# Optimization experiments

Hardware: AMD Instinct MI355X
Metric: run time of the kernel (lower is better)

The kernel has to match this reference:

```python
import jax, jax.numpy as jnp
import numpy as np

N = 20000      # num nodes
E = 200000     # num edges (no self loops; GATConv adds them)
ND = 128       # node_feature_dim
ED = 64        # edge_feature_dim
H = 256        # hidden_dim (= GAT out_channels per head, concat=False)
HEADS = 4
L = 3          # num_gnn_layers


def setup_inputs() -> dict:
    key = jax.random.key(0)
    ks = jax.random.split(key, 24)
    rng = np.random.default_rng(0)
    src = rng.integers(0, N, size=E)
    dst = (src + 1 + rng.integers(0, N - 1, size=E)) % N  # guaranteed no self loops
    edge_index = jnp.asarray(np.stack([src, dst]), dtype=jnp.int32)
    s = 0.05
    inp = {
        'node_features': jax.random.normal(ks[0], (N, ND), jnp.float32),
        'edge_attr': jax.random.normal(ks[1], (E, ED), jnp.float32),
        'enc_w': jax.random.normal(ks[2], (ND, H), jnp.float32) * s,
        'enc_b': jnp.zeros((H,), jnp.float32),
        'edge_enc_w': jax.random.normal(ks[3], (L, ED, H), jnp.float32) * s,
        'edge_enc_b': jnp.zeros((L, H), jnp.float32),
        'gat_w': jax.random.normal(ks[4], (L, H, HEADS * H), jnp.float32) * s,
        'att_src': jax.random.normal(ks[5], (L, HEADS, H), jnp.float32) * s,
        'att_dst': jax.random.normal(ks[6], (L, HEADS, H), jnp.float32) * s,
        'att_edge': jax.random.normal(ks[7], (L, HEADS, H), jnp.float32) * s,
        'lin_edge_w': jax.random.normal(ks[8], (L, 1, HEADS * H), jnp.float32) * s,
        'gat_b': jnp.zeros((L, H), jnp.float32),
        'ln_g': jnp.ones((L, H), jnp.float32),
        'ln_b': jnp.zeros((L, H), jnp.float32),
        'head_w1': jax.random.normal(ks[9], (4, H, H // 2), jnp.float32) * s,
        'head_b1': jnp.zeros((4, H // 2), jnp.float32),
        'head_w2': jax.random.normal(ks[10], (4, H // 2, 1), jnp.float32) * s,
        'head_b2': jnp.zeros((4, 1), jnp.float32),
        'edge_index': edge_index,
    }
    return inp


def _layernorm(x, g, b, eps=1e-5):
    mu = x.mean(-1, keepdims=True)
    v = ((x - mu) ** 2).mean(-1, keepdims=True)
    return g * (x - mu) / jnp.sqrt(v + eps) + b


def _gat_layer(x, src, dst, ew_full, w, a_s_vec, a_d_vec, a_e_vec, lew, bias):
    # x: [N,H]; GATConv(heads=4, concat=False) with scalar edge feature (edge_dim=1)
    xp = (x @ w).reshape(N, HEADS, H)                       # [N,HEADS,H]
    a_s = (xp * a_s_vec).sum(-1)                            # [N,HEADS]
    a_d = (xp * a_d_vec).sum(-1)                            # [N,HEADS]
    ef = (ew_full[:, None] @ lew).reshape(-1, HEADS, H)     # [Etot,HEADS,H]
    a_e = (ef * a_e_vec).sum(-1)                            # [Etot,HEADS]
    logits = jax.nn.leaky_relu(a_s[src] + a_d[dst] + a_e, 0.2)
    m = jax.ops.segment_max(logits, dst, num_segments=N)    # segment softmax over dst
    p = jnp.exp(logits - m[dst])
    ssum = jax.ops.segment_sum(p, dst, num_segments=N)
    alpha = p / ssum[dst]                                   # [Etot,HEADS]
    out = jax.ops.segment_sum(alpha[:, :, None] * xp[src], dst, num_segments=N)
    return out.mean(1) + bias                               # concat=False -> mean over heads


def reference(node_features, edge_attr, enc_w, enc_b, edge_enc_w, edge_enc_b,
              gat_w, att_src, att_dst, att_edge, lin_edge_w, gat_b,
              ln_g, ln_b, head_w1, head_b1, head_w2, head_b2, edge_index):
    src0, dst0 = edge_index[0], edge_index[1]
    loop = jnp.arange(N, dtype=edge_index.dtype)
    src = jnp.concatenate([src0, loop])   # self loops appended (GATConv add_self_loops)
    dst = jnp.concatenate([dst0, loop])
    deg = jax.ops.segment_sum(jnp.ones((E,), node_features.dtype), dst0, num_segments=N)

    x = jax.nn.relu(node_features @ enc_w + enc_b)          # node encoder (dropout: eval)
    for l in range(L):
        ew = (edge_attr @ edge_enc_w[l] + edge_enc_b[l]).mean(-1)  # [E] scalar edge weight
        loop_w = jax.ops.segment_sum(ew, dst0, num_segments=N) / jnp.maximum(deg, 1.0)
        ew_full = jnp.concatenate([ew, loop_w])             # fill_value='mean' for self loops
        h = _gat_layer(x, src, dst, ew_full, gat_w[l], att_src[l], att_dst[l],
                       att_edge[l], lin_edge_w[l], gat_b[l])
        h = _layernorm(h, ln_g[l], ln_b[l])
        x = jax.nn.relu(x + h)
    emb = x                                                 # [N,H]

    # 4 prediction heads vectorized: k in {attrition, engagement, collaboration, anomaly}
    hmid = jax.nn.relu(jnp.einsum('nd,kdh->knh', emb, head_w1) + head_b1[:, None, :])
    o = jnp.einsum('knh,kho->kno', hmid, head_w2) + head_b2[:, None, :]  # [4,N,1]
    attrition = jax.nn.sigmoid(o[0])
    engagement = o[1]
    collaboration = o[2]
    anomaly = jax.nn.sigmoid(o[3])
    return (attrition, engagement, collaboration, anomaly, emb)
```

## Files before the change

### kernel.cpp

```cpp
#include <hip/hip_runtime.h>
#include <math.h>

#define N_NODES 20000
#define N_EDGES 200000
#define NDIM 128
#define EDIM 64
#define HDIM 256
#define HEADS 4
#define NH 1024
#define NLAYERS 3

typedef __attribute__((ext_vector_type(8))) short short8;
typedef __attribute__((ext_vector_type(4))) float floatx4;

__device__ __forceinline__ float b2f(unsigned short u) {
    union { unsigned u; float f; } c; c.u = ((unsigned)u) << 16; return c.f;
}
__device__ __forceinline__ float b2f_lo(unsigned u) {
    union { unsigned u; float f; } c; c.u = u << 16; return c.f;
}
__device__ __forceinline__ float b2f_hi(unsigned u) {
    union { unsigned u; float f; } c; c.u = u & 0xffff0000u; return c.f;
}
__device__ __forceinline__ unsigned short f2b(float f) {
    union { float f; unsigned u; } c; c.f = f;
    unsigned u = c.u;
    return (unsigned short)((u + 0x7FFFu + ((u >> 16) & 1u)) >> 16);
}
__device__ __forceinline__ float lrelu(float v) { return v > 0.f ? v : 0.2f * v; }

__global__ void hist_kernel(const int* __restrict__ dst0, int* __restrict__ cnt) {
    int e = blockIdx.x * 256 + threadIdx.x;
    if (e < N_EDGES) atomicAdd(&cnt[dst0[e]], 1);
}

__global__ __launch_bounds__(1024) void scan_full(const int* __restrict__ cnt,
                                                  int* __restrict__ row_ptr) {
    const int PER = 20;
    __shared__ int wtot[16];
    int t = threadIdx.x, lane = t & 63, wid = t >> 6;
    int base = t * PER;
    int loc[PER];
    int s = 0;
    #pragma unroll
    for (int i = 0; i < PER; i++) {
        int idx = base + i;
        int v = (idx < N_NODES) ? cnt[idx] : 0;
        loc[i] = s; s += v;
    }
    int inc = s;
    #pragma unroll
    for (int off = 1; off < 64; off <<= 1) {
        int tt = __shfl_up(inc, off, 64);
        if (lane >= off) inc += tt;
    }
    if (lane == 63) wtot[wid] = inc;
    __syncthreads();
    int woff = 0;
    #pragma unroll
    for (int w = 0; w < 16; w++) if (w < wid) woff += wtot[w];
    int excl = woff + inc - s;
    #pragma unroll
    for (int i = 0; i < PER; i++) {
        int idx = base + i;
        if (idx < N_NODES) row_ptr[idx] = excl + loc[i];
    }
    if (t == 1023) row_ptr[N_NODES] = excl + s;
}

__global__ __launch_bounds__(256) void fill_ew(const int* __restrict__ src0,
                                               const int* __restrict__ dst0,
                                               const float* __restrict__ edge_attr,
                                               const float* __restrict__ wmean3,
                                               const float* __restrict__ scal3,
                                               const int* __restrict__ row_ptr,
                                               int* __restrict__ fillc,
                                               int* __restrict__ srcCSR,
                                               float* __restrict__ ewCSR4) {
    int e = blockIdx.x * 256 + threadIdx.x;
    if (e >= N_EDGES) return;
    int d = dst0[e];
    int p = atomicAdd(&fillc[d], 1);
    int pos = row_ptr[d] + p;
    srcCSR[pos] = src0[e];
    const float* row = edge_attr + (size_t)e * EDIM;
    float s0 = 0.f, s1 = 0.f, s2 = 0.f;
    #pragma unroll
    for (int dd = 0; dd < EDIM; dd += 4) {
        float4 a  = *(const float4*)(row + dd);
        float4 w0 = *(const float4*)(wmean3 + dd);
        float4 w1 = *(const float4*)(wmean3 + 64 + dd);
        float4 w2 = *(const float4*)(wmean3 + 128 + dd);
        s0 += a.x * w0.x + a.y * w0.y + a.z * w0.z + a.w * w0.w;
        s1 += a.x * w1.x + a.y * w1.y + a.z * w1.z + a.w * w1.w;
        s2 += a.x * w2.x + a.y * w2.y + a.z * w2.z + a.w * w2.w;
    }
    *(float4*)(ewCSR4 + (size_t)pos * 4) =
        make_float4(s0 + scal3[4], s1 + scal3[12], s2 + scal3[20], 0.f);
}

#define PC_CONV   2500
#define PC_TENC   (PC_CONV + 32)
#define PC_GWP    (PC_TENC + 768)
#define PC_WSP    (PC_GWP + 12)
#define PC_THW1   (PC_WSP + 128)
#define PC_TOTAL  (PC_THW1 + 3)

__device__ void transpose_body(const float* in, unsigned short* out, int K, int Nn,
                               int bx, int by, float sh[32][33], float scale) {
    int tid = threadIdx.x;
    int tx = tid & 31, ty = tid >> 5;
    int kb = by * 32, nb = bx * 32;
    #pragma unroll
    for (int i = 0; i < 32; i += 8)
        sh[ty + i][tx] = in[(size_t)(kb + ty + i) * Nn + nb + tx];
    __syncthreads();
    #pragma unroll
    for (int i = 0; i < 32; i += 8)
        out[(size_t)(nb + ty + i) * K + kb + tx] = f2b(scale * sh[tx][ty + i]);
}

__global__ __launch_bounds__(256) void prep_combo(
    const float* __restrict__ node_features, unsigned short* __restrict__ nf_bf,
    const float* __restrict__ enc_w, unsigned short* __restrict__ enc_wt,
    const float* __restrict__ gat_w, unsigned short* __restrict__ gw2t,
    const float* __restrict__ att_src, const float* __restrict__ att_dst,
    float* __restrict__ ws_s, float* __restrict__ ws_d,
    const float* __restrict__ head_w1, unsigned short* __restrict__ hw1t,
    const float* __restrict__ edge_enc_w, const float* __restrict__ edge_enc_b,
    const float* __restrict__ lin_edge_w, const float* __restrict__ att_edge,
    float* __restrict__ wmean3, float* __restrict__ scal3)
{
    __shared__ float sh[32][33];
    int b = blockIdx.x;
    int tid = threadIdx.x;
    if (b < PC_CONV) {
        int i = b * 256 + tid;
        float4 v = ((const float4*)node_features)[i];
        ushort4 o;
        o.x = f2b(v.x); o.y = f2b(v.y); o.z = f2b(v.z); o.w = f2b(v.w);
        ((ushort4*)nf_bf)[i] = o;
    } else if (b < PC_TENC) {
        int b2 = b - PC_CONV;
        transpose_body(enc_w, enc_wt, NDIM, HDIM, b2 & 7, b2 >> 3, sh, 1.f);
    } else if (b < PC_GWP) {
        int b3 = b - PC_TENC;
        int bx = b3 & 7, by = (b3 >> 3) & 7, z = b3 >> 6;
        int l = z >> 2, h = z & 3;
        const float* src = gat_w + (size_t)l * HDIM * NH + (size_t)h * HDIM;
        unsigned short* dst = gw2t + (size_t)l * HDIM * NH + (size_t)h * HDIM;
        int tx = tid & 31, ty = tid >> 5;
        int kb = by * 32, db = bx * 32;
        #pragma unroll
        for (int i = 0; i < 32; i += 8)
            sh[ty + i][tx] = src[(size_t)(kb + ty + i) * NH + db + tx];
        __syncthreads();
        #pragma unroll
        for (int i = 0; i < 32; i += 8)
            dst[(size_t)(db + ty + i) * NH + kb + tx] = f2b(0.25f * sh[tx][ty + i]);
    } else if (b < PC_WSP) {
        int bx = b - PC_GWP;
        int l = bx >> 2, h = bx & 3;
        int k = tid;
        const float* wrow = gat_w + (size_t)l * HDIM * NH + (size_t)k * NH + h * HDIM;
        const float* as = att_src + (size_t)l * NH + h * HDIM;
        const float* ad = att_dst + (size_t)l * NH + h * HDIM;
        float s1 = 0.f, s2 = 0.f;
        for (int d = 0; d < HDIM; d += 4) {
            float4 w4 = *(const float4*)(wrow + d);
            float4 a4 = *(const float4*)(as + d);
            float4 b4 = *(const float4*)(ad + d);
            s1 += w4.x * a4.x + w4.y * a4.y + w4.z * a4.z + w4.w * a4.w;
            s2 += w4.x * b4.x + w4.y * b4.y + w4.z * b4.z + w4.w * b4.w;
        }
        ws_s[(size_t)bx * HDIM + k] = s1;
        ws_d[(size_t)bx * HDIM + k] = s2;
    } else if (b < PC_THW1) {
        int b4 = b - PC_WSP;
        int bx = b4 & 3, by = (b4 >> 2) & 7, z = b4 >> 5;
        transpose_body(head_w1 + (size_t)z * HDIM * 128,
                       hw1t + (size_t)z * 128 * HDIM, HDIM, 128, bx, by, sh, 1.f);
    } else {
        int l = b - PC_THW1;
        const float* eew = edge_enc_w + (size_t)l * EDIM * HDIM;
        const float* eeb = edge_enc_b + (size_t)l * HDIM;
        const float* lew = lin_edge_w + (size_t)l * NH;
        const float* ae  = att_edge + (size_t)l * NH;
        float* wm = wmean3 + l * 64;
        float* sc = scal3 + l * 8;
        if (tid < 64) {
            float s = 0.f;
            for (int d = 0; d < HDIM; d++) s += eew[tid * HDIM + d];
            wm[tid] = s * (1.f / HDIM);
        } else if (tid < 68) {
            int h = tid - 64;
            float s = 0.f;
            for (int d = 0; d < HDIM; d++) s += lew[h * HDIM + d] * ae[h * HDIM + d];
            sc[h] = s;
        } else if (tid == 68) {
            float s = 0.f;
            for (int d = 0; d < HDIM; d++) s += eeb[d];
            sc[4] = s * (1.f / HDIM);
        }
    }
}

template <bool RELU, bool BIAS>
__global__ __launch_bounds__(256) void gemm_bf16(
    const unsigned short* __restrict__ A, const unsigned short* __restrict__ Bt,
    const float* __restrict__ bias, unsigned short* __restrict__ C,
    int M, int Ntot, int K)
{
    __shared__ char lds[24576];
    unsigned short* As = (unsigned short*)lds;
    unsigned short* Bs = (unsigned short*)(lds + 8192);
    unsigned short* Cs = (unsigned short*)lds;

    int Cb = Ntot >> 7;
    int P  = (M + 63) >> 6;
    int d  = blockIdx.x;
    int xcd = d & 7;
    int i5  = d >> 3;
    int p   = xcd + 8 * (i5 / Cb);
    int cblk = i5 % Cb;
    if (p >= P) return;
    int row0 = p * 64;
    int col0 = cblk * 128;

    int tid = threadIdx.x;
    int lane = tid & 63;
    int wid = tid >> 6;
    int wm = (wid >> 1) * 32;
    int wn = (wid & 1) * 64;
    int lm = lane & 15;
    int q8 = (lane >> 4) * 8;
    int q4 = (lane >> 4) * 4;

    floatx4 acc[2][4];
    #pragma unroll
    for (int i = 0; i < 2; i++)
        #pragma unroll
        for (int j = 0; j < 4; j++)
            acc[i][j] = (floatx4)(0.f);

    int arow = tid >> 2;
    int acol = (tid & 3) * 8;
    int garow = row0 + arow; if (garow > M - 1) garow = M - 1;

    for (int k0 = 0; k0 < K; k0 += 64) {
        #pragma unroll
        for (int kk = 0; kk < 2; kk++) {
            int kb = k0 + kk * 32;
            __builtin_amdgcn_global_load_lds(
                (__attribute__((address_space(1))) const void*)(A + (size_t)garow * K + kb + acol),
                (__attribute__((address_space(3))) void*)(As + kk * 2048 + tid * 8), 16, 0, 0);
            #pragma unroll
            for (int r = 0; r < 2; r++) {
                int chunk = tid + r * 256;
                int brow = chunk >> 2;
                int bcol = (chunk & 3) * 8;
                __builtin_amdgcn_global_load_lds(
                    (__attribute__((address_space(1))) const void*)(Bt + (size_t)(col0 + brow) * K + kb + bcol),
                    (__attribute__((address_space(3))) void*)(Bs + kk * 4096 + chunk * 8), 16, 0, 0);
            }
        }
        __syncthreads();
        #pragma unroll
        for (int kk = 0; kk < 2; kk++) {
            short8 af[2], bf[4];
            #pragma unroll
            for (int i = 0; i < 2; i++)
                af[i] = *(const short8*)(As + kk * 2048 + (wm + i * 16 + lm) * 32 + q8);
            #pragma unroll
            for (int j = 0; j < 4; j++)
                bf[j] = *(const short8*)(Bs + kk * 4096 + (wn + j * 16 + lm) * 32 + q8);
            #pragma unroll
            for (int i = 0; i < 2; i++)
                #pragma unroll
                for (int j = 0; j < 4; j++)
                    acc[i][j] = __builtin_amdgcn_mfma_f32_16x16x32_bf16(af[i], bf[j], acc[i][j], 0, 0, 0);
        }
        __syncthreads();
    }

    #pragma unroll
    for (int i = 0; i < 2; i++) {
        #pragma unroll
        for (int j = 0; j < 4; j++) {
            int cl = wn + j * 16 + lm;
            float bv = BIAS ? bias[col0 + cl] : 0.f;
            #pragma unroll
            for (int reg = 0; reg < 4; reg++) {
                int rl = wm + i * 16 + q4 + reg;
                float v = acc[i][j][reg];
                if (BIAS) v += bv;
                if (RELU) v = fmaxf(v, 0.f);
                Cs[rl * 128 + cl] = f2b(v);
            }
        }
    }
    __syncthreads();
    int row = tid >> 2;
    int seg = (tid & 3) * 32;
    if (row0 + row < M) {
        #pragma unroll
        for (int u = 0; u < 4; u++) {
            int4 v = *(const int4*)(Cs + row * 128 + seg + u * 8);
            *(int4*)(C + (size_t)(row0 + row) * Ntot + col0 + seg + u * 8) = v;
        }
    }
}

__global__ __launch_bounds__(256) void gemm_head(
    const unsigned short* __restrict__ A, const unsigned short* __restrict__ Bt,
    const float* __restrict__ bias, int M, int Ntot, int K,
    const float* __restrict__ w2, const float* __restrict__ b2v,
    float* __restrict__ outp)
{
    __shared__ char lds[24576];
    unsigned short* As = (unsigned short*)lds;
    unsigned short* Bs = (unsigned short*)(lds + 8192);
    unsigned short* Cs = (unsigned short*)lds;

    int Cb = Ntot >> 7;
    int P  = (M + 63) >> 6;
    int d  = blockIdx.x;
    int xcd = d & 7;
    int i5  = d >> 3;
    int p   = xcd + 8 * (i5 / Cb);
    int cblk = i5 % Cb;
    if (p >= P) return;
    int row0 = p * 64;
    int col0 = cblk * 128;

    int tid = threadIdx.x;
    int lane = tid & 63;
    int wid = tid >> 6;
    int wm = (wid >> 1) * 32;
    int wn = (wid & 1) * 64;
    int lm = lane & 15;
    int q8 = (lane >> 4) * 8;
    int q4 = (lane >> 4) * 4;

    floatx4 acc[2][4];
    #pragma unroll
    for (int i = 0; i < 2; i++)
        #pragma unroll
        for (int j = 0; j < 4; j++)
            acc[i][j] = (floatx4)(0.f);

    int arow = tid >> 2;
    int acol = (tid & 3) * 8;
    int garow = row0 + arow; if (garow > M - 1) garow = M - 1;

    for (int k0 = 0; k0 < K; k0 += 64) {
        #pragma unroll
        for (int kk = 0; kk < 2; kk++) {
            int kb = k0 + kk * 32;
            __builtin_amdgcn_global_load_lds(
                (__attribute__((address_space(1))) const void*)(A + (size_t)garow * K + kb + acol),
                (__attribute__((address_space(3))) void*)(As + kk * 2048 + tid * 8), 16, 0, 0);
            #pragma unroll
            for (int r = 0; r < 2; r++) {
                int chunk = tid + r * 256;
                int brow = chunk >> 2;
                int bcol = (chunk & 3) * 8;
                __builtin_amdgcn_global_load_lds(
                    (__attribute__((address_space(1))) const void*)(Bt + (size_t)(col0 + brow) * K + kb + bcol),
                    (__attribute__((address_space(3))) void*)(Bs + kk * 4096 + chunk * 8), 16, 0, 0);
            }
        }
        __syncthreads();
        #pragma unroll
        for (int kk = 0; kk < 2; kk++) {
            short8 af[2], bf[4];
            #pragma unroll
            for (int i = 0; i < 2; i++)
                af[i] = *(const short8*)(As + kk * 2048 + (wm + i * 16 + lm) * 32 + q8);
            #pragma unroll
            for (int j = 0; j < 4; j++)
                bf[j] = *(const short8*)(Bs + kk * 4096 + (wn + j * 16 + lm) * 32 + q8);
            #pragma unroll
            for (int i = 0; i < 2; i++)
                #pragma unroll
                for (int j = 0; j < 4; j++)
                    acc[i][j] = __builtin_amdgcn_mfma_f32_16x16x32_bf16(af[i], bf[j], acc[i][j], 0, 0, 0);
        }
        __syncthreads();
    }

    #pragma unroll
    for (int i = 0; i < 2; i++) {
        #pragma unroll
        for (int j = 0; j < 4; j++) {
            int cl = wn + j * 16 + lm;
            float bv = bias[col0 + cl];
            #pragma unroll
            for (int reg = 0; reg < 4; reg++) {
                int rl = wm + i * 16 + q4 + reg;
                float v = fmaxf(acc[i][j][reg] + bv, 0.f);
                Cs[rl * 128 + cl] = f2b(v);
            }
        }
    }
    __syncthreads();
    int row = tid >> 2;
    int seg = (tid & 3) * 32;
    int k = col0 >> 7;
    const float* wr = w2 + k * 128;
    const unsigned short* cr = Cs + row * 128 + seg;
    float s = 0.f;
    #pragma unroll
    for (int u = 0; u < 4; u++) {
        int4 v = *(const int4*)(cr + u * 8);
        float4 w0 = *(const float4*)(wr + seg + u * 8);
        float4 w1 = *(const float4*)(wr + seg + u * 8 + 4);
        s += b2f_lo((unsigned)v.x) * w0.x + b2f_hi((unsigned)v.x) * w0.y
           + b2f_lo((unsigned)v.y) * w0.z + b2f_hi((unsigned)v.y) * w0.w;
        s += b2f_lo((unsigned)v.z) * w1.x + b2f_hi((unsigned)v.z) * w1.y
           + b2f_lo((unsigned)v.w) * w1.z + b2f_hi((unsigned)v.w) * w1.w;
    }
    s += __shfl_xor(s, 1, 64);
    s += __shfl_xor(s, 2, 64);
    if ((tid & 3) == 0 && row0 + row < M) {
        s += b2v[k];
        if (k == 0 || k == 3) s = 1.f / (1.f + __expf(-s));
        outp[(size_t)k * N_NODES + row0 + row] = s;
    }
}

__global__ __launch_bounds__(256) void attn_x(const unsigned short* __restrict__ x_bf,
                                              const float* __restrict__ ws_s,
                                              const float* __restrict__ ws_d,
                                              float* __restrict__ a_s,
                                              float* __restrict__ a_d)
{
    int wid = threadIdx.x >> 6, lane = threadIdx.x & 63;
    int n = blockIdx.x * 4 + wid;
    ushort4 xv = *(const ushort4*)(x_bf + (size_t)n * HDIM + lane * 4);
    float x0 = b2f(xv.x), x1 = b2f(xv.y), x2 = b2f(xv.z), x3 = b2f(xv.w);
    float ss[4], sd[4];
    #pragma unroll
    for (int h = 0; h < 4; h++) {
        float4 s4 = *(const float4*)(ws_s + h * HDIM + lane * 4);
        float4 d4 = *(const float4*)(ws_d + h * HDIM + lane * 4);
        ss[h] = x0 * s4.x + x1 * s4.y + x2 * s4.z + x3 * s4.w;
        sd[h] = x0 * d4.x + x1 * d4.y + x2 * d4.z + x3 * d4.w;
    }
    #pragma unroll
    for (int off = 32; off > 0; off >>= 1)
        #pragma unroll
        for (int h = 0; h < 4; h++) {
            ss[h] += __shfl_xor(ss[h], off, 64);
            sd[h] += __shfl_xor(sd[h], off, 64);
        }
    if (lane == 0) {
        *(float4*)(a_s + n * 4) = make_float4(ss[0], ss[1], ss[2], ss[3]);
        *(float4*)(a_d + n * 4) = make_float4(sd[0], sd[1], sd[2], sd[3]);
    }
}

__global__ __launch_bounds__(256) void gat_agg_fused(
    const unsigned short* __restrict__ x_bf, const float* __restrict__ a_s,
    const float* __restrict__ a_d,
    const float* __restrict__ scal, const int* __restrict__ row_ptr,
    const int* __restrict__ srcCSR, const float* __restrict__ ewCSR4,
    int l, unsigned short* __restrict__ agg)
{
    int wid = threadIdx.x >> 6, lane = threadIdx.x & 63;
    int n = blockIdx.x * 4 + wid;
    int r0 = row_ptr[n];
    int deg = row_ptr[n + 1] - r0;
    int cnt = deg + 1;

    float4 c4 = *(const float4*)scal;
    float4 as4 = *(const float4*)(a_s + (size_t)n * 4);
    float4 ad4 = *(const float4*)(a_d + (size_t)n * 4);

    int sv0 = n; float w0 = 0.f;
    if (lane < deg) {
        sv0 = srcCSR[r0 + lane];
        w0 = ewCSR4[(((size_t)(r0 + lane)) << 2) + l];
    }
    float sw = w0;
    for (int c0 = 64; c0 < deg; c0 += 64) {
        int i2 = c0 + lane;
        if (i2 < deg) sw += ewCSR4[(((size_t)(r0 + i2)) << 2) + l];
    }
    #pragma unroll
    for (int off = 32; off > 0; off >>= 1) sw += __shfl_xor(sw, off, 64);
    float lw = sw / fmaxf((float)deg, 1.f);

    float4 zself;
    zself.x = lrelu(as4.x + ad4.x + c4.x * lw);
    zself.y = lrelu(as4.y + ad4.y + c4.y * lw);
    zself.z = lrelu(as4.z + ad4.z + c4.z * lw);
    zself.w = lrelu(as4.w + ad4.w + c4.w * lw);

    auto comp_z = [&](int c0, int& sv, float4& z) {
        int ix = c0 + lane;
        if (ix < deg) {
            sv = srcCSR[r0 + ix];
            float w = ewCSR4[(((size_t)(r0 + ix)) << 2) + l];
            float4 zs = *(const float4*)(a_s + (size_t)sv * 4);
            z.x = lrelu(zs.x + ad4.x + c4.x * w);
            z.y = lrelu(zs.y + ad4.y + c4.y * w);
            z.z = lrelu(zs.z + ad4.z + c4.z * w);
            z.w = lrelu(zs.w + ad4.w + c4.w * w);
        } else if (ix == deg) {
            sv = n; z = zself;
        } else {
            sv = n; z.x = z.y = z.z = z.w = -1e30f;
        }
    };

    float4 z0;
    if (lane < deg) {
        float4 zs = *(const float4*)(a_s + (size_t)sv0 * 4);
        z0.x = lrelu(zs.x + ad4.x + c4.x * w0);
        z0.y = lrelu(zs.y + ad4.y + c4.y * w0);
        z0.z = lrelu(zs.z + ad4.z + c4.z * w0);
        z0.w = lrelu(zs.w + ad4.w + c4.w * w0);
    } else if (lane == deg) {
        z0 = zself;
    } else {
        z0.x = z0.y = z0.z = z0.w = -1e30f;
    }

    float4 p0;
    p0.x = __expf(z0.x); p0.y = __expf(z0.y);
    p0.z = __expf(z0.z); p0.w = __expf(z0.w);
    float s0 = p0.x, s1 = p0.y, s2 = p0.z, s3 = p0.w;
    for (int c0 = 64; c0 < cnt; c0 += 64) {
        int sv; float4 z; comp_z(c0, sv, z);
        s0 += __expf(z.x); s1 += __expf(z.y);
        s2 += __expf(z.z); s3 += __expf(z.w);
    }
    #pragma unroll
    for (int off = 32; off > 0; off >>= 1) {
        s0 += __shfl_xor(s0, off, 64);
        s1 += __shfl_xor(s1, off, 64);
        s2 += __shfl_xor(s2, off, 64);
        s3 += __shfl_xor(s3, off, 64);
    }
    float i0 = 1.f / s0, i1 = 1.f / s1, i2 = 1.f / s2, i3 = 1.f / s3;
    float4 al0;
    al0.x = p0.x * i0; al0.y = p0.y * i1; al0.z = p0.z * i2; al0.w = p0.w * i3;

    float acc[4][4] = {};
    const unsigned short* xw = x_bf + (size_t)lane * 4;

    auto acc_one = [&](uint2 u, float a0, float a1, float a2, float a3) {
        float x0 = b2f_lo(u.x), x1 = b2f_hi(u.x), x2 = b2f_lo(u.y), x3 = b2f_hi(u.y);
        acc[0][0] += a0 * x0; acc[0][1] += a0 * x1; acc[0][2] += a0 * x2; acc[0][3] += a0 * x3;
        acc[1][0] += a1 * x0; acc[1][1] += a1 * x1; acc[1][2] += a1 * x2; acc[1][3] += a1 * x3;
        acc[2][0] += a2 * x0; acc[2][1] += a2 * x1; acc[2][2] += a2 * x2; acc[2][3] += a2 * x3;
        acc[3][0] += a3 * x0; acc[3][1] += a3 * x1; acc[3][2] += a3 * x2; acc[3][3] += a3 * x3;
    };

    auto agg_chunk = [&](int sv, float4 al, int mc) {
        int j = 0;
        for (; j + 3 < mc; j += 4) {
            int sA = __builtin_amdgcn_readfirstlane(__shfl(sv, j, 64));
            int sB = __builtin_amdgcn_readfirstlane(__shfl(sv, j + 1, 64));
            int sC = __builtin_amdgcn_readfirstlane(__shfl(sv, j + 2, 64));
            int sD = __builtin_amdgcn_readfirstlane(__shfl(sv, j + 3, 64));
            uint2 uA = *(const uint2*)(xw + (size_t)sA * HDIM);
            uint2 uB = *(const uint2*)(xw + (size_t)sB * HDIM);
            uint2 uC = *(const uint2*)(xw + (size_t)sC * HDIM);
            uint2 uD = *(const uint2*)(xw + (size_t)sD * HDIM);
            acc_one(uA, __shfl(al.x, j, 64), __shfl(al.y, j, 64),
                        __shfl(al.z, j, 64), __shfl(al.w, j, 64));
            acc_one(uB, __shfl(al.x, j + 1, 64), __shfl(al.y, j + 1, 64),
                        __shfl(al.z, j + 1, 64), __shfl(al.w, j + 1, 64));
            acc_one(uC, __shfl(al.x, j + 2, 64), __shfl(al.y, j + 2, 64),
                        __shfl(al.z, j + 2, 64), __shfl(al.w, j + 2, 64));
            acc_one(uD, __shfl(al.x, j + 3, 64), __shfl(al.y, j + 3, 64),
                        __shfl(al.z, j + 3, 64), __shfl(al.w, j + 3, 64));
        }
        for (; j + 1 < mc; j += 2) {
            int sA = __builtin_amdgcn_readfirstlane(__shfl(sv, j, 64));
            int sB = __builtin_amdgcn_readfirstlane(__shfl(sv, j + 1, 64));
            uint2 uA = *(const uint2*)(xw + (size_t)sA * HDIM);
            uint2 uB = *(const uint2*)(xw + (size_t)sB * HDIM);
            acc_one(uA, __shfl(al.x, j, 64), __shfl(al.y, j, 64),
                        __shfl(al.z, j, 64), __shfl(al.w, j, 64));
            acc_one(uB, __shfl(al.x, j + 1, 64), __shfl(al.y, j + 1, 64),
                        __shfl(al.z, j + 1, 64), __shfl(al.w, j + 1, 64));
        }
        if (j < mc) {
            int sA = __builtin_amdgcn_readfirstlane(__shfl(sv, j, 64));
            uint2 uA = *(const uint2*)(xw + (size_t)sA * HDIM);
            acc_one(uA, __shfl(al.x, j, 64), __shfl(al.y, j, 64),
                        __shfl(al.z, j, 64), __shfl(al.w, j, 64));
        }
    };

    agg_chunk(sv0, al0, min(64, cnt));
    for (int c0 = 64; c0 < cnt; c0 += 64) {
        int sv; float4 z; comp_z(c0, sv, z);
        float4 al;
        al.x = __expf(z.x) * i0; al.y = __expf(z.y) * i1;
        al.z = __expf(z.z) * i2; al.w = __expf(z.w) * i3;
        agg_chunk(sv, al, min(64, cnt - c0));
    }

    unsigned short* ag = agg + (size_t)n * NH + lane * 4;
    #pragma unroll
    for (int h = 0; h < 4; h++) {
        ushort4 o;
        o.x = f2b(acc[h][0]); o.y = f2b(acc[h][1]);
        o.z = f2b(acc[h][2]); o.w = f2b(acc[h][3]);
        *(ushort4*)(ag + h * 256) = o;
    }
}

template <bool ATTN, bool EMB>
__global__ __launch_bounds__(256) void ln_residual(const unsigned short* __restrict__ y_bf,
                                                   const float* __restrict__ ln_g,
                                                   const float* __restrict__ ln_b,
                                                   unsigned short* __restrict__ x_bf,
                                                   const float* __restrict__ ws_s,
                                                   const float* __restrict__ ws_d,
                                                   float* __restrict__ a_s,
                                                   float* __restrict__ a_d,
                                                   float* __restrict__ emb_out)
{
    int n = blockIdx.x * 4 + (threadIdx.x >> 6);
    int lane = threadIdx.x & 63;
    ushort4 yv = *(const ushort4*)(y_bf + (size_t)n * HDIM + lane * 4);
    float y0 = b2f(yv.x), y1 = b2f(yv.y), y2 = b2f(yv.z), y3 = b2f(yv.w);
    float s1 = y0 + y1 + y2 + y3;
    float s2 = y0 * y0 + y1 * y1 + y2 * y2 + y3 * y3;
    #pragma unroll
    for (int off = 32; off > 0; off >>= 1) {
        s1 += __shfl_xor(s1, off, 64);
        s2 += __shfl_xor(s2, off, 64);
    }
    float mu = s1 * (1.f / HDIM);
    float var = s2 * (1.f / HDIM) - mu * mu;
    float rsig = rsqrtf(var + 1e-5f);
    float4 g = *(const float4*)(ln_g + lane * 4);
    float4 b = *(const float4*)(ln_b + lane * 4);
    ushort4 xv = *(const ushort4*)(x_bf + (size_t)n * HDIM + lane * 4);
    ushort4 o;
    o.x = f2b(fmaxf(b2f(xv.x) + g.x * (y0 - mu) * rsig + b.x, 0.f));
    o.y = f2b(fmaxf(b2f(xv.y) + g.y * (y1 - mu) * rsig + b.y, 0.f));
    o.z = f2b(fmaxf(b2f(xv.z) + g.z * (y2 - mu) * rsig + b.z, 0.f));
    o.w = f2b(fmaxf(b2f(xv.w) + g.w * (y3 - mu) * rsig + b.w, 0.f));
    *(ushort4*)(x_bf + (size_t)n * HDIM + lane * 4) = o;

    float xn0 = b2f(o.x), xn1 = b2f(o.y), xn2 = b2f(o.z), xn3 = b2f(o.w);
    if (EMB) {
        *(float4*)(emb_out + (size_t)n * HDIM + lane * 4) = make_float4(xn0, xn1, xn2, xn3);
    }
    if (ATTN) {
        float ss[4], sd[4];
        #pragma unroll
        for (int h = 0; h < 4; h++) {
            float4 s4 = *(const float4*)(ws_s + h * HDIM + lane * 4);
            float4 d4 = *(const float4*)(ws_d + h * HDIM + lane * 4);
            ss[h] = xn0 * s4.x + xn1 * s4.y + xn2 * s4.z + xn3 * s4.w;
            sd[h] = xn0 * d4.x + xn1 * d4.y + xn2 * d4.z + xn3 * d4.w;
        }
        #pragma unroll
        for (int off = 32; off > 0; off >>= 1)
            #pragma unroll
            for (int h = 0; h < 4; h++) {
                ss[h] += __shfl_xor(ss[h], off, 64);
                sd[h] += __shfl_xor(sd[h], off, 64);
            }
        if (lane == 0) {
            *(float4*)(a_s + n * 4) = make_float4(ss[0], ss[1], ss[2], ss[3]);
            *(float4*)(a_d + n * 4) = make_float4(sd[0], sd[1], sd[2], sd[3]);
        }
    }
}

extern "C" void kernel_launch(void* const* d_in, const int* in_sizes, int n_in,
                              void* d_out, int out_size, void* d_ws, size_t ws_size,
                              hipStream_t stream) {
    const float* node_features = (const float*)d_in[0];
    const float* edge_attr     = (const float*)d_in[1];
    const float* enc_w         = (const float*)d_in[2];
    const float* enc_b         = (const float*)d_in[3];
    const float* edge_enc_w    = (const float*)d_in[4];
    const float* edge_enc_b    = (const float*)d_in[5];
    const float* gat_w         = (const float*)d_in[6];
    const float* att_src       = (const float*)d_in[7];
    const float* att_dst       = (const float*)d_in[8];
    const float* att_edge      = (const float*)d_in[9];
    const float* lin_edge_w    = (const float*)d_in[10];
    const float* gat_b         = (const float*)d_in[11];
    const float* ln_g          = (const float*)d_in[12];
    const float* ln_b          = (const float*)d_in[13];
    const float* head_w1       = (const float*)d_in[14];
    const float* head_b1       = (const float*)d_in[15];
    const float* head_w2       = (const float*)d_in[16];
    const float* head_b2       = (const float*)d_in[17];
    const int*   edge_index    = (const int*)d_in[18];
    const int* src0 = edge_index;
    const int* dst0 = edge_index + N_EDGES;
    float* out = (float*)d_out;

    char* cur = (char*)d_ws;
    auto alloc = [&](size_t bytes) { char* p = cur; cur += (bytes + 255) & ~(size_t)255; return p; };
    unsigned short* x_bf   = (unsigned short*)alloc((size_t)N_NODES * HDIM * 2);
    unsigned short* agg    = (unsigned short*)alloc((size_t)N_NODES * NH * 2);
    unsigned short* y_bf   = (unsigned short*)alloc((size_t)N_NODES * HDIM * 2);
    unsigned short* nf_bf  = (unsigned short*)alloc((size_t)N_NODES * NDIM * 2);
    unsigned short* enc_wt = (unsigned short*)alloc((size_t)HDIM * NDIM * 2);
    unsigned short* gw2t   = (unsigned short*)alloc((size_t)NLAYERS * NH * HDIM * 2);
    unsigned short* hw1t   = (unsigned short*)alloc((size_t)512 * HDIM * 2);
    float* ws_s   = (float*)alloc((size_t)NLAYERS * 4 * HDIM * 4);
    float* ws_d   = (float*)alloc((size_t)NLAYERS * 4 * HDIM * 4);
    float* a_s    = (float*)alloc((size_t)N_NODES * 4 * 4);
    float* a_d    = (float*)alloc((size_t)N_NODES * 4 * 4);
    float* ewCSR4 = (float*)alloc((size_t)N_EDGES * 4 * 4);
    float* wmean3 = (float*)alloc(192 * 4);
    float* scal3  = (float*)alloc(24 * 4);
    int* cnt      = (int*)alloc((size_t)2 * N_NODES * 4);
    int* fillc    = cnt + N_NODES;
    int* row_ptr  = (int*)alloc((size_t)(N_NODES + 1) * 4);
    int* srcCSR   = (int*)alloc((size_t)N_EDGES * 4);

    hipMemsetAsync(cnt, 0, (size_t)2 * N_NODES * sizeof(int), stream);

    prep_combo<<<PC_TOTAL, 256, 0, stream>>>(
        node_features, nf_bf, enc_w, enc_wt, gat_w, gw2t, att_src, att_dst,
        ws_s, ws_d, head_w1, hw1t, edge_enc_w, edge_enc_b, lin_edge_w, att_edge,
        wmean3, scal3);
    hist_kernel<<<(N_EDGES + 255) / 256, 256, 0, stream>>>(dst0, cnt);
    scan_full<<<1, 1024, 0, stream>>>(cnt, row_ptr);
    fill_ew<<<(N_EDGES + 255) / 256, 256, 0, stream>>>(src0, dst0, edge_attr, wmean3, scal3,
                                                       row_ptr, fillc, srcCSR, ewCSR4);

    const int GEMM_GRID_256 = 8 * (((N_NODES + 63) / 64 + 7) / 8) * (256 / 128);
    const int GRID_HEAD = 8 * (((N_NODES + 63) / 64 + 7) / 8) * (512 / 128);

    gemm_bf16<true, true><<<GEMM_GRID_256, 256, 0, stream>>>(
        nf_bf, enc_wt, enc_b, x_bf, N_NODES, HDIM, NDIM);
    attn_x<<<N_NODES / 4, 256, 0, stream>>>(x_bf, ws_s, ws_d, a_s, a_d);

    for (int l = 0; l < NLAYERS; l++) {
        gat_agg_fused<<<N_NODES / 4, 256, 0, stream>>>(
            x_bf, a_s, a_d, scal3 + l * 8, row_ptr, srcCSR, ewCSR4, l, agg);
        gemm_bf16<false, true><<<GEMM_GRID_256, 256, 0, stream>>>(
            agg, gw2t + (size_t)l * NH * HDIM, gat_b + (size_t)l * HDIM, y_bf,
            N_NODES, HDIM, NH);
        if (l < NLAYERS - 1) {
            ln_residual<true, false><<<N_NODES / 4, 256, 0, stream>>>(
                y_bf, ln_g + (size_t)l * HDIM, ln_b + (size_t)l * HDIM, x_bf,
                ws_s + (size_t)(l + 1) * 4 * HDIM, ws_d + (size_t)(l + 1) * 4 * HDIM,
                a_s, a_d, nullptr);
        } else {
            ln_residual<false, true><<<N_NODES / 4, 256, 0, stream>>>(
                y_bf, ln_g + (size_t)l * HDIM, ln_b + (size_t)l * HDIM, x_bf,
                nullptr, nullptr, nullptr, nullptr, out + 4 * N_NODES);
        }
    }

    gemm_head<<<GRID_HEAD, 256, 0, stream>>>(
        x_bf, hw1t, head_b1, N_NODES, 512, HDIM, head_w2, head_b2, out);
}
```

Before: 413.6 us.

## Assign each destination node to a half-wavefront with 16-byte gathers in GAT aggregation

```diff
diff --git a/kernel.cpp b/kernel.cpp
--- a/kernel.cpp
+++ b/kernel.cpp
@@ -467,28 +467,28 @@
     const int* __restrict__ srcCSR, const float* __restrict__ ewCSR4,
     int l, unsigned short* __restrict__ agg)
 {
-    int wid = threadIdx.x >> 6, lane = threadIdx.x & 63;
-    int n = blockIdx.x * 4 + wid;
+    int sub = threadIdx.x & 31;
+    int hw  = threadIdx.x >> 5;
+    int n = blockIdx.x * 8 + hw;
     int r0 = row_ptr[n];
     int deg = row_ptr[n + 1] - r0;
     int cnt = deg + 1;
+    int cntMax = max(cnt, __shfl_xor(cnt, 32, 64));
 
     float4 c4 = *(const float4*)scal;
     float4 as4 = *(const float4*)(a_s + (size_t)n * 4);
     float4 ad4 = *(const float4*)(a_d + (size_t)n * 4);
 
     int sv0 = n; float w0 = 0.f;
-    if (lane < deg) {
-        sv0 = srcCSR[r0 + lane];
-        w0 = ewCSR4[(((size_t)(r0 + lane)) << 2) + l];
+    if (sub < deg) {
+        sv0 = srcCSR[r0 + sub];
+        w0 = ewCSR4[(((size_t)(r0 + sub)) << 2) + l];
     }
     float sw = w0;
-    for (int c0 = 64; c0 < deg; c0 += 64) {
-        int i2 = c0 + lane;
-        if (i2 < deg) sw += ewCSR4[(((size_t)(r0 + i2)) << 2) + l];
-    }
-    #pragma unroll
-    for (int off = 32; off > 0; off >>= 1) sw += __shfl_xor(sw, off, 64);
+    for (int i = 32 + sub; i < deg; i += 32)
+        sw += ewCSR4[(((size_t)(r0 + i)) << 2) + l];
+    #pragma unroll
+    for (int off = 16; off > 0; off >>= 1) sw += __shfl_xor(sw, off, 32);
     float lw = sw / fmaxf((float)deg, 1.f);
 
     float4 zself;
@@ -498,7 +498,7 @@
     zself.w = lrelu(as4.w + ad4.w + c4.w * lw);
 
     auto comp_z = [&](int c0, int& sv, float4& z) {
-        int ix = c0 + lane;
+        int ix = c0 + sub;
         if (ix < deg) {
             sv = srcCSR[r0 + ix];
             float w = ewCSR4[(((size_t)(r0 + ix)) << 2) + l];
@@ -515,13 +515,13 @@
     };
 
     float4 z0;
-    if (lane < deg) {
+    if (sub < deg) {
         float4 zs = *(const float4*)(a_s + (size_t)sv0 * 4);
         z0.x = lrelu(zs.x + ad4.x + c4.x * w0);
         z0.y = lrelu(zs.y + ad4.y + c4.y * w0);
         z0.z = lrelu(zs.z + ad4.z + c4.z * w0);
         z0.w = lrelu(zs.w + ad4.w + c4.w * w0);
-    } else if (lane == deg) {
+    } else if (sub == deg) {
         z0 = zself;
     } else {
         z0.x = z0.y = z0.z = z0.w = -1e30f;
@@ -531,87 +531,96 @@
     p0.x = __expf(z0.x); p0.y = __expf(z0.y);
     p0.z = __expf(z0.z); p0.w = __expf(z0.w);
     float s0 = p0.x, s1 = p0.y, s2 = p0.z, s3 = p0.w;
-    for (int c0 = 64; c0 < cnt; c0 += 64) {
+    for (int c0 = 32; c0 < cnt; c0 += 32) {
         int sv; float4 z; comp_z(c0, sv, z);
         s0 += __expf(z.x); s1 += __expf(z.y);
         s2 += __expf(z.z); s3 += __expf(z.w);
     }
     #pragma unroll
-    for (int off = 32; off > 0; off >>= 1) {
-        s0 += __shfl_xor(s0, off, 64);
-        s1 += __shfl_xor(s1, off, 64);
-        s2 += __shfl_xor(s2, off, 64);
-        s3 += __shfl_xor(s3, off, 64);
+    for (int off = 16; off > 0; off >>= 1) {
+        s0 += __shfl_xor(s0, off, 32);
+        s1 += __shfl_xor(s1, off, 32);
+        s2 += __shfl_xor(s2, off, 32);
+        s3 += __shfl_xor(s3, off, 32);
     }
     float i0 = 1.f / s0, i1 = 1.f / s1, i2 = 1.f / s2, i3 = 1.f / s3;
     float4 al0;
     al0.x = p0.x * i0; al0.y = p0.y * i1; al0.z = p0.z * i2; al0.w = p0.w * i3;
 
-    float acc[4][4] = {};
-    const unsigned short* xw = x_bf + (size_t)lane * 4;
-
-    auto acc_one = [&](uint2 u, float a0, float a1, float a2, float a3) {
-        float x0 = b2f_lo(u.x), x1 = b2f_hi(u.x), x2 = b2f_lo(u.y), x3 = b2f_hi(u.y);
-        acc[0][0] += a0 * x0; acc[0][1] += a0 * x1; acc[0][2] += a0 * x2; acc[0][3] += a0 * x3;
-        acc[1][0] += a1 * x0; acc[1][1] += a1 * x1; acc[1][2] += a1 * x2; acc[1][3] += a1 * x3;
-        acc[2][0] += a2 * x0; acc[2][1] += a2 * x1; acc[2][2] += a2 * x2; acc[2][3] += a2 * x3;
-        acc[3][0] += a3 * x0; acc[3][1] += a3 * x1; acc[3][2] += a3 * x2; acc[3][3] += a3 * x3;
+    float acc[4][8] = {};
+    const unsigned short* xw = x_bf + (size_t)sub * 8;
+
+    auto acc_one = [&](uint4 u, float a0, float a1, float a2, float a3) {
+        float xv[8];
+        xv[0] = b2f_lo(u.x); xv[1] = b2f_hi(u.x);
+        xv[2] = b2f_lo(u.y); xv[3] = b2f_hi(u.y);
+        xv[4] = b2f_lo(u.z); xv[5] = b2f_hi(u.z);
+        xv[6] = b2f_lo(u.w); xv[7] = b2f_hi(u.w);
+        #pragma unroll
+        for (int e = 0; e < 8; e++) {
+            acc[0][e] += a0 * xv[e];
+            acc[1][e] += a1 * xv[e];
+            acc[2][e] += a2 * xv[e];
+            acc[3][e] += a3 * xv[e];
+        }
     };
 
     auto agg_chunk = [&](int sv, float4 al, int mc) {
         int j = 0;
         for (; j + 3 < mc; j += 4) {
-            int sA = __builtin_amdgcn_readfirstlane(__shfl(sv, j, 64));
-            int sB = __builtin_amdgcn_readfirstlane(__shfl(sv, j + 1, 64));
-            int sC = __builtin_amdgcn_readfirstlane(__shfl(sv, j + 2, 64));
-            int sD = __builtin_amdgcn_readfirstlane(__shfl(sv, j + 3, 64));
-            uint2 uA = *(const uint2*)(xw + (size_t)sA * HDIM);
-            uint2 uB = *(const uint2*)(xw + (size_t)sB * HDIM);
-            uint2 uC = *(const uint2*)(xw + (size_t)sC * HDIM);
-            uint2 uD = *(const uint2*)(xw + (size_t)sD * HDIM);
-            acc_one(uA, __shfl(al.x, j, 64), __shfl(al.y, j, 64),
-                        __shfl(al.z, j, 64), __shfl(al.w, j, 64));
-            acc_one(uB, __shfl(al.x, j + 1, 64), __shfl(al.y, j + 1, 64),
-                        __shfl(al.z, j + 1, 64), __shfl(al.w, j + 1, 64));
-            acc_one(uC, __shfl(al.x, j + 2, 64), __shfl(al.y, j + 2, 64),
-                        __shfl(al.z, j + 2, 64), __shfl(al.w, j + 2, 64));
-            acc_one(uD, __shfl(al.x, j + 3, 64), __shfl(al.y, j + 3, 64),
-                        __shfl(al.z, j + 3, 64), __shfl(al.w, j + 3, 64));
+            int sA = __shfl(sv, j, 32);
+            int sB = __shfl(sv, j + 1, 32);
+            int sC = __shfl(sv, j + 2, 32);
+            int sD = __shfl(sv, j + 3, 32);
+            uint4 uA = *(const uint4*)(xw + (size_t)sA * HDIM);
+            uint4 uB = *(const uint4*)(xw + (size_t)sB * HDIM);
+            uint4 uC = *(const uint4*)(xw + (size_t)sC * HDIM);
+            uint4 uD = *(const uint4*)(xw + (size_t)sD * HDIM);
+            acc_one(uA, __shfl(al.x, j, 32), __shfl(al.y, j, 32),
+                        __shfl(al.z, j, 32), __shfl(al.w, j, 32));
+            acc_one(uB, __shfl(al.x, j + 1, 32), __shfl(al.y, j + 1, 32),
+                        __shfl(al.z, j + 1, 32), __shfl(al.w, j + 1, 32));
+            acc_one(uC, __shfl(al.x, j + 2, 32), __shfl(al.y, j + 2, 32),
+                        __shfl(al.z, j + 2, 32), __shfl(al.w, j + 2, 32));
+            acc_one(uD, __shfl(al.x, j + 3, 32), __shfl(al.y, j + 3, 32),
+                        __shfl(al.z, j + 3, 32), __shfl(al.w, j + 3, 32));
         }
         for (; j + 1 < mc; j += 2) {
-            int sA = __builtin_amdgcn_readfirstlane(__shfl(sv, j, 64));
-            int sB = __builtin_amdgcn_readfirstlane(__shfl(sv, j + 1, 64));
-            uint2 uA = *(const uint2*)(xw + (size_t)sA * HDIM);
-            uint2 uB = *(const uint2*)(xw + (size_t)sB * HDIM);
-            acc_one(uA, __shfl(al.x, j, 64), __shfl(al.y, j, 64),
-                        __shfl(al.z, j, 64), __shfl(al.w, j, 64));
-            acc_one(uB, __shfl(al.x, j + 1, 64), __shfl(al.y, j + 1, 64),
-                        __shfl(al.z, j + 1, 64), __shfl(al.w, j + 1, 64));
+            int sA = __shfl(sv, j, 32);
+            int sB = __shfl(sv, j + 1, 32);
+            uint4 uA = *(const uint4*)(xw + (size_t)sA * HDIM);
+            uint4 uB = *(const uint4*)(xw + (size_t)sB * HDIM);
+            acc_one(uA, __shfl(al.x, j, 32), __shfl(al.y, j, 32),
+                        __shfl(al.z, j, 32), __shfl(al.w, j, 32));
+            acc_one(uB, __shfl(al.x, j + 1, 32), __shfl(al.y, j + 1, 32),
+                        __shfl(al.z, j + 1, 32), __shfl(al.w, j + 1, 32));
         }
         if (j < mc) {
-            int sA = __builtin_amdgcn_readfirstlane(__shfl(sv, j, 64));
-            uint2 uA = *(const uint2*)(xw + (size_t)sA * HDIM);
-            acc_one(uA, __shfl(al.x, j, 64), __shfl(al.y, j, 64),
-                        __shfl(al.z, j, 64), __shfl(al.w, j, 64));
+            int sA = __shfl(sv, j, 32);
+            uint4 uA = *(const uint4*)(xw + (size_t)sA * HDIM);
+            acc_one(uA, __shfl(al.x, j, 32), __shfl(al.y, j, 32),
+                        __shfl(al.z, j, 32), __shfl(al.w, j, 32));
         }
     };
 
-    agg_chunk(sv0, al0, min(64, cnt));
-    for (int c0 = 64; c0 < cnt; c0 += 64) {
+    agg_chunk(sv0, al0, min(32, cntMax));
+    for (int c0 = 32; c0 < cntMax; c0 += 32) {
         int sv; float4 z; comp_z(c0, sv, z);
         float4 al;
         al.x = __expf(z.x) * i0; al.y = __expf(z.y) * i1;
         al.z = __expf(z.z) * i2; al.w = __expf(z.w) * i3;
-        agg_chunk(sv, al, min(64, cnt - c0));
-    }
-
-    unsigned short* ag = agg + (size_t)n * NH + lane * 4;
+        agg_chunk(sv, al, min(32, cntMax - c0));
+    }
+
+    unsigned short* ag = agg + (size_t)n * NH + sub * 8;
     #pragma unroll
     for (int h = 0; h < 4; h++) {
-        ushort4 o;
-        o.x = f2b(acc[h][0]); o.y = f2b(acc[h][1]);
-        o.z = f2b(acc[h][2]); o.w = f2b(acc[h][3]);
-        *(ushort4*)(ag + h * 256) = o;
+        uint4 o;
+        o.x = (unsigned)f2b(acc[h][0]) | ((unsigned)f2b(acc[h][1]) << 16);
+        o.y = (unsigned)f2b(acc[h][2]) | ((unsigned)f2b(acc[h][3]) << 16);
+        o.z = (unsigned)f2b(acc[h][4]) | ((unsigned)f2b(acc[h][5]) << 16);
+        o.w = (unsigned)f2b(acc[h][6]) | ((unsigned)f2b(acc[h][7]) << 16);
+        *(uint4*)(ag + h * 256) = o;
     }
 }
 
@@ -743,7 +752,7 @@
     attn_x<<<N_NODES / 4, 256, 0, stream>>>(x_bf, ws_s, ws_d, a_s, a_d);
 
     for (int l = 0; l < NLAYERS; l++) {
-        gat_agg_fused<<<N_NODES / 4, 256, 0, stream>>>(
+        gat_agg_fused<<<N_NODES / 8, 256, 0, stream>>>(
             x_bf, a_s, a_d, scal3 + l * 8, row_ptr, srcCSR, ewCSR4, l, agg);
         gemm_bf16<false, true><<<GEMM_GRID_256, 256, 0, stream>>>(
             agg, gw2t + (size_t)l * NH * HDIM, gat_b + (size_t)l * HDIM, y_bf,
```

Measured after the change: 1.199 ms. +189.8%, slower.
